# Kernel optimization log

Measured on AMD Instinct MI355X. Metric: run time of the kernel, lower is better.

Reference implementation:

```python
import jax, jax.numpy as jnp
import numpy as np

B, T, M, DFEAT = 256, 30, 2, 256
D_MODEL, NHEAD, NLAYERS, DFF = 768, 12, 12, 3072


def _pe(max_len, d):
    # sinusoidal positional encoding buffer (deterministic, matches PositionalEncoding)
    pos = np.arange(max_len, dtype=np.float32)[:, None]
    div = np.exp(np.arange(0, d, 2, dtype=np.float32) * (-np.log(10000.0) / d))
    pe = np.zeros((max_len, d), dtype=np.float32)
    pe[:, 0::2] = np.sin(pos * div)
    pe[:, 1::2] = np.cos(pos * div)
    return jnp.asarray(pe)


def setup_inputs() -> dict:
    key = jax.random.key(0)
    ks = jax.random.split(key, 16)
    n = lambda k, shape: jax.random.normal(k, shape, jnp.float32) * 0.02
    inp = {}
    inp['x'] = jax.random.normal(ks[0], (B, T, M, DFEAT), jnp.float32)
    inp['mask'] = jax.random.randint(ks[1], (B, T), 0, 2) > 0
    inp['Wp'] = n(ks[2], (D_MODEL, DFEAT)); inp['bp'] = jnp.zeros((D_MODEL,), jnp.float32)
    inp['mod_emb'] = n(ks[3], (M, D_MODEL)); inp['day_emb'] = n(ks[4], (T, D_MODEL))
    inp['readmit'] = n(ks[5], (D_MODEL,)); inp['contrast'] = n(ks[6], (D_MODEL,))
    inp['WqkvS'] = n(ks[7], (NLAYERS, 3 * D_MODEL, D_MODEL)); inp['bqkvS'] = jnp.zeros((NLAYERS, 3 * D_MODEL), jnp.float32)
    inp['WoS'] = n(ks[8], (NLAYERS, D_MODEL, D_MODEL)); inp['boS'] = jnp.zeros((NLAYERS, D_MODEL), jnp.float32)
    inp['ln1wS'] = jnp.ones((NLAYERS, D_MODEL), jnp.float32); inp['ln1bS'] = jnp.zeros((NLAYERS, D_MODEL), jnp.float32)
    inp['ln2wS'] = jnp.ones((NLAYERS, D_MODEL), jnp.float32); inp['ln2bS'] = jnp.zeros((NLAYERS, D_MODEL), jnp.float32)
    inp['W1S'] = n(ks[9], (NLAYERS, DFF, D_MODEL)); inp['b1S'] = jnp.zeros((NLAYERS, DFF), jnp.float32)
    inp['W2S'] = n(ks[10], (NLAYERS, D_MODEL, DFF)); inp['b2S'] = jnp.zeros((NLAYERS, D_MODEL), jnp.float32)
    inp['hW1'] = n(ks[11], (D_MODEL // 2, D_MODEL)); inp['hb1'] = jnp.zeros((D_MODEL // 2,), jnp.float32)
    inp['hlnw'] = jnp.ones((D_MODEL // 2,), jnp.float32); inp['hlnb'] = jnp.zeros((D_MODEL // 2,), jnp.float32)
    inp['hW2'] = n(ks[12], (1, D_MODEL // 2)); inp['hb2'] = jnp.zeros((1,), jnp.float32)
    return inp


def _ln(z, w, b):
    m = z.mean(-1, keepdims=True)
    v = ((z - m) ** 2).mean(-1, keepdims=True)
    return (z - m) * jax.lax.rsqrt(v + 1e-5) * w + b


def reference(x, mask, Wp, bp, mod_emb, day_emb, readmit, contrast,
              WqkvS, bqkvS, WoS, boS, ln1wS, ln1bS, ln2wS, ln2bS,
              W1S, b1S, W2S, b2S, hW1, hb1, hlnw, hlnb, hW2, hb2):
    Bb, Tt, Mm, _ = x.shape
    d = Wp.shape[0]; H = NHEAD; dh = d // H
    L = Tt * Mm; S = L + 2  # static padded length (valid positions key-masked, so faithful)
    # project + activation + modality/day embeddings
    x_flat = x.reshape(Bb, L, -1)
    x_emb = jax.nn.gelu(jnp.einsum('bld,kd->blk', x_flat, Wp) + bp, approximate=False)
    mod_ids = jnp.tile(jnp.arange(Mm), Tt)
    day_ids = jnp.repeat(jnp.arange(Tt), Mm)
    x_emb = x_emb + mod_emb[mod_ids] + day_emb[day_ids]
    # vectorized ragged pack: valid tokens to the front (stable argsort replaces python loop)
    is_valid = jnp.repeat(mask, Mm, axis=1)  # [B, L]
    vlen = is_valid.sum(axis=1).astype(jnp.int32)
    order = jnp.argsort(jnp.logical_not(is_valid).astype(jnp.int32), axis=1, stable=True)
    packed = jnp.take_along_axis(x_emb, order[:, :, None], axis=1)
    packed = packed * (jnp.arange(L)[None, :, None] < vlen[:, None, None])
    h = jnp.pad(packed, ((0, 0), (0, 2), (0, 0)))
    # special tokens at positions vlen / vlen+1, with positional encoding added only there
    pe = _pe(S, d)
    bidx = jnp.arange(Bb)
    h = h.at[bidx, vlen].set(readmit + pe[vlen])
    h = h.at[bidx, vlen + 1].set(contrast + pe[vlen + 1])
    # key padding mask -> additive attention bias
    pad = jnp.arange(S)[None, :] > (vlen[:, None] + 1)
    attn_bias = jnp.where(pad, -1e9, 0.0).astype(h.dtype)[:, None, None, :]

    def layer(hc, p):
        Wqkv, bqkv, Wo, bo, l1w, l1b, l2w, l2b, W1, b1, W2, b2 = p
        z = _ln(hc, l1w, l1b)  # pre-LN
        qkv = jnp.einsum('bsd,kd->bsk', z, Wqkv) + bqkv
        q, k, v = jnp.split(qkv, 3, axis=-1)
        q = q.reshape(Bb, S, H, dh).transpose(0, 2, 1, 3)
        k = k.reshape(Bb, S, H, dh).transpose(0, 2, 1, 3)
        v = v.reshape(Bb, S, H, dh).transpose(0, 2, 1, 3)
        sc = jnp.einsum('bhqd,bhkd->bhqk', q, k) / (dh ** 0.5) + attn_bias
        a = jax.nn.softmax(sc, axis=-1)
        o = jnp.einsum('bhqk,bhkd->bhqd', a, v).transpose(0, 2, 1, 3).reshape(Bb, S, d)
        hc = hc + jnp.einsum('bsd,kd->bsk', o, Wo) + bo
        z2 = _ln(hc, l2w, l2b)
        ff = jax.nn.gelu(jnp.einsum('bsd,fd->bsf', z2, W1) + b1, approximate=False)
        hc = hc + jnp.einsum('bsf,df->bsd', ff, W2) + b2
        return hc, None

    h, _ = jax.lax.scan(layer, h, (WqkvS, bqkvS, WoS, boS, ln1wS, ln1bS, ln2wS, ln2bS, W1S, b1S, W2S, b2S))
    # readmit token readout + MLP head
    tok = h[bidx, vlen]
    hm = jax.nn.gelu(_ln(tok @ hW1.T + hb1, hlnw, hlnb), approximate=False)
    logits = (hm @ hW2.T + hb2)[:, 0]
    return logits
```

## Files before the change

kernel.cpp:

```cpp
#include <hip/hip_runtime.h>
#include <hip/hip_bf16.h>
#include <cmath>

#define BB 256
#define TT 30
#define SS 62
#define DM 768
#define NH 12
#define DFF 3072
#define NTOK (BB*SS)

typedef unsigned short us16;
typedef __bf16 bf16x8 __attribute__((ext_vector_type(8)));
typedef float f32x4 __attribute__((ext_vector_type(4)));

__device__ __forceinline__ us16 f2b(float f){ __hip_bfloat16 t=__float2bfloat16(f); return *reinterpret_cast<us16*>(&t); }
__device__ __forceinline__ float b2f(us16 u){ __hip_bfloat16 t; *reinterpret_cast<us16*>(&t)=u; return __bfloat162float(t); }
__device__ __forceinline__ float dgelu(float x){ return 0.5f*x*(1.0f+erff(x*0.7071067811865475f)); }
__device__ __forceinline__ f32x4 mfma16(bf16x8 a, bf16x8 b, f32x4 c){ return __builtin_amdgcn_mfma_f32_16x16x32_bf16(a,b,c,0,0,0); }

__device__ __forceinline__ void gload16(const void* g, void* l) {
    __builtin_amdgcn_global_load_lds(
        (__attribute__((address_space(1))) void*)(uintptr_t)g,
        (__attribute__((address_space(3))) void*)(uint32_t)(uintptr_t)l,
        16, 0, 0);
}

__global__ __launch_bounds__(256) void detect_mask_kernel(
    const unsigned char* __restrict__ m, int* __restrict__ flag)
{
    __shared__ int sub4, oddw;
    if (threadIdx.x == 0) { sub4 = 0; oddw = 0; }
    __syncthreads();
    for (int j = threadIdx.x; j < BB*TT; j += blockDim.x) {
        unsigned char v = m[j];
        if (v) {
            if (j & 3) sub4 = 1;
            if ((j >> 2) & 1) oddw = 1;
        }
    }
    __syncthreads();
    if (threadIdx.x == 0) *flag = sub4 ? 1 : (oddw ? 0 : 2);
}

__global__ __launch_bounds__(256) void cvt_kernel(
    const float* __restrict__ in, us16* __restrict__ out, int n8)
{
    int t = blockIdx.x*256 + threadIdx.x;
    if (t >= n8) return;
    const float4* s = (const float4*)(in + (long)t*8);
    float4 a = s[0], b = s[1];
    us16 tmp[8] = {f2b(a.x),f2b(a.y),f2b(a.z),f2b(a.w),f2b(b.x),f2b(b.y),f2b(b.z),f2b(b.w)};
    *(uint4*)(out + (long)t*8) = *(uint4*)tmp;
}

__global__ __launch_bounds__(256) void cvt_layer_kernel(
    const float* __restrict__ qkv, const float* __restrict__ wo,
    const float* __restrict__ w1,  const float* __restrict__ w2,
    us16* __restrict__ dqkv, us16* __restrict__ dwo,
    us16* __restrict__ dw1,  us16* __restrict__ dw2)
{
    long t = (long)blockIdx.x*256 + threadIdx.x;
    const float* src; us16* dst; long off;
    if (t < 221184)      { src = qkv; dst = dqkv; off = t; }
    else if (t < 294912) { src = wo;  dst = dwo;  off = t - 221184; }
    else if (t < 589824) { src = w1;  dst = dw1;  off = t - 294912; }
    else                 { src = w2;  dst = dw2;  off = t - 589824; }
    const float4* s = (const float4*)(src + off*8);
    float4 a = s[0], b = s[1];
    us16 tmp[8] = {f2b(a.x),f2b(a.y),f2b(a.z),f2b(a.w),f2b(b.x),f2b(b.y),f2b(b.z),f2b(b.w)};
    *(uint4*)(dst + off*8) = *(uint4*)tmp;
}

template<int EPI>
__global__ __launch_bounds__(256) void gemm_bf(const us16* __restrict__ A,
    const us16* __restrict__ W, const float* __restrict__ bias,
    void* __restrict__ outv, int N, int K, int ntn)
{
    __shared__ us16 As[2][128*64];
    __shared__ us16 Ws[2][128*64];
    const int tid  = threadIdx.x;
    const int lane = tid & 63;
    const int wave = tid >> 6;
    const int wr = wave >> 1, wc = wave & 1;
    const int li = lane & 15, g = lane >> 4;

    const int nwg = gridDim.x;
    const int lin = blockIdx.x;
    const int newlin = (lin & 7) * (nwg >> 3) + (lin >> 3);
    const long tm = newlin / ntn, tn = newlin % ntn;

    const int swzc = ((lane & 7) ^ (lane >> 3)) * 8;
    const us16* agp = A + (tm*128 + wave*32 + (lane>>3))*(long)K + swzc;
    const us16* wgp = W + (tn*128 + wave*32 + (lane>>3))*(long)K + swzc;

    f32x4 acc[4][4];
    #pragma unroll
    for (int i=0;i<4;i++)
        #pragma unroll
        for (int j=0;j<4;j++)
            #pragma unroll
            for (int r=0;r<4;r++) acc[i][j][r] = 0.f;

    const int nt = K >> 6;
    #pragma unroll
    for (int c=0;c<4;c++) {
        gload16(agp + (long)c*8*K, &As[0][(wave*4+c)*512]);
        gload16(wgp + (long)c*8*K, &Ws[0][(wave*4+c)*512]);
    }
    __syncthreads();

    int cur = 0;
    for (int t = 0; t < nt; ++t) {
        if (t + 1 < nt) {
            const long k0 = (long)(t+1) * 64;
            #pragma unroll
            for (int c=0;c<4;c++) {
                gload16(agp + k0 + (long)c*8*K, &As[cur^1][(wave*4+c)*512]);
                gload16(wgp + k0 + (long)c*8*K, &Ws[cur^1][(wave*4+c)*512]);
            }
        }
        #pragma unroll
        for (int kk=0; kk<2; kk++) {
            bf16x8 afr[4], bfr[4];
            #pragma unroll
            for (int mi=0;mi<4;mi++) {
                int r = wr*64 + mi*16 + li;
                afr[mi] = *(const bf16x8*)&As[cur][r*64 + ((kk*4 + g) ^ (r & 7))*8];
            }
            #pragma unroll
            for (int ni=0;ni<4;ni++) {
                int r = wc*64 + ni*16 + li;
                bfr[ni] = *(const bf16x8*)&Ws[cur][r*64 + ((kk*4 + g) ^ (r & 7))*8];
            }
            #pragma unroll
            for (int mi=0;mi<4;mi++)
                #pragma unroll
                for (int ni=0;ni<4;ni++)
                    acc[mi][ni] = mfma16(afr[mi], bfr[ni], acc[mi][ni]);
        }
        __syncthreads();
        cur ^= 1;
    }

    const long rbase = tm*128 + wr*64 + (g*4);
    const long cbase = tn*128 + wc*64 + li;
    #pragma unroll
    for (int mi=0;mi<4;mi++) {
        #pragma unroll
        for (int ni=0;ni<4;ni++) {
            long col = cbase + ni*16;
            float bv = bias[col];
            #pragma unroll
            for (int r=0;r<4;r++) {
                long row = rbase + mi*16 + r;
                float v = acc[mi][ni][r] + bv;
                if constexpr (EPI == 0) {
                    ((us16*)outv)[row*(long)N + col] = f2b(v);
                } else if constexpr (EPI == 1) {
                    ((us16*)outv)[row*(long)N + col] = f2b(dgelu(v));
                } else {
                    float* o = (float*)outv;
                    o[row*(long)N + col] += v;
                }
            }
        }
    }
}

__global__ __launch_bounds__(256) void pack_kernel(
    const us16* __restrict__ e, const void* __restrict__ maskv,
    const int* __restrict__ flagp,
    const float* __restrict__ mod_emb, const float* __restrict__ day_emb,
    const float* __restrict__ readmit, const float* __restrict__ contrast,
    float* __restrict__ h, int* __restrict__ vlen_out)
{
    __shared__ int day_of[TT];
    __shared__ int nvalid;
    const int b = blockIdx.x, tid = threadIdx.x;
    if (tid == 0) {
        const int fl = *flagp;
        int c = 0;
        for (int t = 0; t < TT; t++) {
            int mv;
            if (fl == 1)      mv = ((const unsigned char*)maskv)[b*TT + t];
            else if (fl == 2) mv = ((const int*)maskv)[(b*TT + t)*2];
            else              mv = ((const int*)maskv)[b*TT + t];
            if (mv != 0) day_of[c++] = t;
        }
        nvalid = c;
        vlen_out[b] = 2*c;
    }
    __syncthreads();
    const int vl = 2*nvalid;
    for (int p = 0; p < SS; p++) {
        for (int d = tid; d < DM; d += 256) {
            float val;
            if (p < vl) {
                int day = day_of[p >> 1];
                int m = p & 1;
                int l = day*2 + m;
                val = b2f(e[((long)b*(TT*2) + l)*DM + d]) + mod_emb[m*DM + d] + day_emb[day*DM + d];
            } else if (p == vl || p == vl + 1) {
                float freq = expf(-(float)(d & ~1) * (9.2103403719761836f/768.f));
                float pe = (d & 1) ? cosf((float)p * freq) : sinf((float)p * freq);
                val = ((p == vl) ? readmit[d] : contrast[d]) + pe;
            } else {
                val = 0.f;
            }
            h[((long)b*SS + p)*DM + d] = val;
        }
    }
}

__global__ __launch_bounds__(256) void ln_kernel(
    const float* __restrict__ x, const float* __restrict__ w,
    const float* __restrict__ bprm, us16* __restrict__ z)
{
    const int row  = blockIdx.x*4 + (threadIdx.x >> 6);
    const int lane = threadIdx.x & 63;
    const float* xr = x + (long)row*DM;
    float4 v[3];
    float s = 0.f, s2 = 0.f;
    #pragma unroll
    for (int j=0;j<3;j++) {
        v[j] = *(const float4*)(xr + lane*4 + j*256);
        s  += v[j].x + v[j].y + v[j].z + v[j].w;
        s2 += v[j].x*v[j].x + v[j].y*v[j].y + v[j].z*v[j].z + v[j].w*v[j].w;
    }
    #pragma unroll
    for (int d=1; d<64; d<<=1) { s += __shfl_xor(s, d); s2 += __shfl_xor(s2, d); }
    const float m  = s * (1.f/768.f);
    const float var = s2 * (1.f/768.f) - m*m;
    const float rs = rsqrtf(var + 1e-5f);
    us16* zr = z + (long)row*DM;
    #pragma unroll
    for (int j=0;j<3;j++) {
        int c0 = lane*4 + j*256;
        float vv[4] = {v[j].x, v[j].y, v[j].z, v[j].w};
        ushort4 o;
        o.x = f2b((vv[0]-m)*rs*w[c0+0] + bprm[c0+0]);
        o.y = f2b((vv[1]-m)*rs*w[c0+1] + bprm[c0+1]);
        o.z = f2b((vv[2]-m)*rs*w[c0+2] + bprm[c0+2]);
        o.w = f2b((vv[3]-m)*rs*w[c0+3] + bprm[c0+3]);
        *(ushort4*)(zr + c0) = o;
    }
}

__global__ __launch_bounds__(256) void attn_kernel(
    const us16* __restrict__ qkv, const int* __restrict__ vlenp,
    us16* __restrict__ ctx)
{
    __shared__ us16 Ql[64*64];
    __shared__ us16 Kl[64*64];
    __shared__ us16 Vt[64*64];
    __shared__ us16 Pl[4*16*64];
    const int b = blockIdx.x, hh = blockIdx.y;
    const int tid = threadIdx.x;
    const int vl = vlenp[b];

    {
        int s  = tid >> 2;
        int d0 = (tid & 3) * 16;
        if (s < SS) {
            long base = ((long)b*SS + s)*(3*DM) + hh*64 + d0;
            uint4 a0 = *(const uint4*)(qkv + base);
            uint4 a1 = *(const uint4*)(qkv + base + 8);
            *(uint4*)&Ql[s*64 + d0]     = a0;
            *(uint4*)&Ql[s*64 + d0 + 8] = a1;
            uint4 c0 = *(const uint4*)(qkv + base + DM);
            uint4 c1 = *(const uint4*)(qkv + base + DM + 8);
            *(uint4*)&Kl[s*64 + d0]     = c0;
            *(uint4*)&Kl[s*64 + d0 + 8] = c1;
            us16 vv[16];
            *(uint4*)&vv[0] = *(const uint4*)(qkv + base + 2*DM);
            *(uint4*)&vv[8] = *(const uint4*)(qkv + base + 2*DM + 8);
            #pragma unroll
            for (int j=0;j<16;j++) Vt[(d0+j)*64 + s] = vv[j];
        } else {
            uint4 zz = make_uint4(0,0,0,0);
            *(uint4*)&Ql[s*64 + d0] = zz; *(uint4*)&Ql[s*64 + d0 + 8] = zz;
            *(uint4*)&Kl[s*64 + d0] = zz; *(uint4*)&Kl[s*64 + d0 + 8] = zz;
            #pragma unroll
            for (int j=0;j<16;j++) Vt[(d0+j)*64 + s] = 0;
        }
    }
    __syncthreads();

    const int lane = tid & 63, wave = tid >> 6;
    const int li = lane & 15, g = lane >> 4;
    const int qbase = wave * 16;

    f32x4 sacc[4];
    #pragma unroll
    for (int kb=0; kb<4; kb++) {
        f32x4 a; a[0]=a[1]=a[2]=a[3]=0.f;
        #pragma unroll
        for (int dc=0; dc<2; dc++) {
            bf16x8 qa = *(const bf16x8*)&Ql[(qbase + li)*64 + dc*32 + g*8];
            bf16x8 ka = *(const bf16x8*)&Kl[(kb*16 + li)*64 + dc*32 + g*8];
            a = mfma16(qa, ka, a);
        }
        sacc[kb] = a;
    }

    float den[4];
    #pragma unroll
    for (int r=0;r<4;r++) {
        float sc[4]; float mx = -3e38f;
        #pragma unroll
        for (int kb=0;kb<4;kb++) {
            int key = kb*16 + li;
            float v = sacc[kb][r]*0.125f + ((key <= vl + 1) ? 0.f : -1e9f);
            sc[kb] = v; mx = fmaxf(mx, v);
        }
        #pragma unroll
        for (int d=1; d<16; d<<=1) mx = fmaxf(mx, __shfl_xor(mx, d));
        float sm = 0.f;
        #pragma unroll
        for (int kb=0;kb<4;kb++) {
            float e = expf(sc[kb] - mx);
            sm += e;
            Pl[wave*1024 + (g*4 + r)*64 + kb*16 + li] = f2b(e);
        }
        #pragma unroll
        for (int d=1; d<16; d<<=1) sm += __shfl_xor(sm, d);
        den[r] = sm;
    }
    __syncthreads();

    #pragma unroll
    for (int vb=0; vb<4; vb++) {
        f32x4 oa; oa[0]=oa[1]=oa[2]=oa[3]=0.f;
        #pragma unroll
        for (int kc=0; kc<2; kc++) {
            bf16x8 pa = *(const bf16x8*)&Pl[wave*1024 + li*64 + kc*32 + g*8];
            bf16x8 va = *(const bf16x8*)&Vt[(vb*16 + li)*64 + kc*32 + g*8];
            oa = mfma16(pa, va, oa);
        }
        #pragma unroll
        for (int r=0;r<4;r++) {
            int s = qbase + g*4 + r;
            if (s < SS)
                ctx[((long)b*SS + s)*DM + hh*64 + vb*16 + li] = f2b(oa[r] / den[r]);
        }
    }
}

__global__ __launch_bounds__(384) void head_kernel(
    const float* __restrict__ h, const int* __restrict__ vlenp,
    const float* __restrict__ hW1, const float* __restrict__ hb1,
    const float* __restrict__ hlnw, const float* __restrict__ hlnb,
    const float* __restrict__ hW2, const float* __restrict__ hb2,
    float* __restrict__ out)
{
    __shared__ float tokS[DM];
    __shared__ float ps[6], ps2[6];
    const int b = blockIdx.x, tid = threadIdx.x;
    const float* tok = h + ((long)b*SS + vlenp[b])*DM;
    for (int i = tid; i < DM; i += 384) tokS[i] = tok[i];
    __syncthreads();

    const float* wrow = hW1 + (long)tid*DM;
    float acc = hb1[tid];
    for (int k = 0; k < DM; k += 4) {
        float4 wv = *(const float4*)(wrow + k);
        acc += tokS[k]*wv.x + tokS[k+1]*wv.y + tokS[k+2]*wv.z + tokS[k+3]*wv.w;
    }
    float s = acc, s2 = acc*acc;
    #pragma unroll
    for (int d=1; d<64; d<<=1) { s += __shfl_xor(s, d); s2 += __shfl_xor(s2, d); }
    const int wavei = tid >> 6, lane = tid & 63;
    if (lane == 0) { ps[wavei] = s; ps2[wavei] = s2; }
    __syncthreads();
    float S = 0.f, S2 = 0.f;
    for (int i=0;i<6;i++){ S += ps[i]; S2 += ps2[i]; }
    const float m = S * (1.f/384.f);
    const float var = S2 * (1.f/384.f) - m*m;
    const float rs = rsqrtf(var + 1e-5f);
    float z = (acc - m)*rs*hlnw[tid] + hlnb[tid];
    float part = dgelu(z) * hW2[tid];
    #pragma unroll
    for (int d=1; d<64; d<<=1) part += __shfl_xor(part, d);
    __syncthreads();
    if (lane == 0) ps[wavei] = part;
    __syncthreads();
    if (tid == 0) {
        float t = 0.f;
        for (int i=0;i<6;i++) t += ps[i];
        out[b] = t + hb2[0];
    }
}

extern "C" void kernel_launch(void* const* d_in, const int* in_sizes, int n_in,
                              void* d_out, int out_size, void* d_ws, size_t ws_size,
                              hipStream_t stream)
{
    (void)in_sizes; (void)n_in; (void)out_size; (void)ws_size;
    const float* x        = (const float*)d_in[0];
    const void*  mask     = d_in[1];
    const float* Wp       = (const float*)d_in[2];
    const float* bp       = (const float*)d_in[3];
    const float* mod_emb  = (const float*)d_in[4];
    const float* day_emb  = (const float*)d_in[5];
    const float* readmit  = (const float*)d_in[6];
    const float* contrast = (const float*)d_in[7];
    const float* WqkvS    = (const float*)d_in[8];
    const float* bqkvS    = (const float*)d_in[9];
    const float* WoS      = (const float*)d_in[10];
    const float* boS      = (const float*)d_in[11];
    const float* ln1w     = (const float*)d_in[12];
    const float* ln1b     = (const float*)d_in[13];
    const float* ln2w     = (const float*)d_in[14];
    const float* ln2b     = (const float*)d_in[15];
    const float* W1S      = (const float*)d_in[16];
    const float* b1S      = (const float*)d_in[17];
    const float* W2S      = (const float*)d_in[18];
    const float* b2S      = (const float*)d_in[19];
    const float* hW1      = (const float*)d_in[20];
    const float* hb1      = (const float*)d_in[21];
    const float* hlnw     = (const float*)d_in[22];
    const float* hlnb     = (const float*)d_in[23];
    const float* hW2      = (const float*)d_in[24];
    const float* hb2      = (const float*)d_in[25];
    float* out = (float*)d_out;

    char* ws = (char*)d_ws;
    float* h    = (float*)ws;
    us16*  zb   = (us16*) (ws + 48758784);
    us16*  big  = (us16*) (ws + 73138176);
    us16*  wl   = (us16*) (ws + 170655744);
    us16*  xb   = (us16*) (ws + 184811520);
    us16*  wpb  = (us16*) (ws + 192675840);
    int*   vlen = (int*)  (ws + 193069056);
    int*   mflag= (int*)  (ws + 193070080);
    us16*  qkvb = big;
    us16*  ffb  = big;
    us16*  eb   = big;
    us16* qkvw = wl;
    us16* wow  = wl + 1769472;
    us16* w1w  = wl + 2359296;
    us16* w2w  = wl + 4718592;

    detect_mask_kernel<<<1,256,0,stream>>>((const unsigned char*)mask, mflag);
    cvt_kernel<<<1920,256,0,stream>>>(x, xb, 491520);
    cvt_kernel<<<96,256,0,stream>>>(Wp, wpb, 24576);
    gemm_bf<1><<<720,256,0,stream>>>(xb, wpb, bp, eb, DM, 256, 6);
    pack_kernel<<<256,256,0,stream>>>(eb, mask, mflag, mod_emb, day_emb, readmit, contrast, h, vlen);

    for (int l = 0; l < 12; l++) {
        cvt_layer_kernel<<<3456,256,0,stream>>>(
            WqkvS + (long)l*3*DM*DM, WoS + (long)l*DM*DM,
            W1S + (long)l*DFF*DM,    W2S + (long)l*DM*DFF,
            qkvw, wow, w1w, w2w);
        ln_kernel<<<NTOK/4,256,0,stream>>>(h, ln1w + l*DM, ln1b + l*DM, zb);
        gemm_bf<0><<<2232,256,0,stream>>>(zb, qkvw, bqkvS + l*3*DM, qkvb, 3*DM, DM, 18);
        attn_kernel<<<dim3(256,12),256,0,stream>>>(qkvb, vlen, zb);
        gemm_bf<2><<<744,256,0,stream>>>(zb, wow, boS + l*DM, h, DM, DM, 6);
        ln_kernel<<<NTOK/4,256,0,stream>>>(h, ln2w + l*DM, ln2b + l*DM, zb);
        gemm_bf<1><<<2976,256,0,stream>>>(zb, w1w, b1S + l*DFF, ffb, DFF, DM, 24);
        gemm_bf<2><<<744,256,0,stream>>>(ffb, w2w, b2S + l*DM, h, DM, DFF, 6);
    }

    head_kernel<<<256,384,0,stream>>>(h, vlen, hW1, hb1, hlnw, hlnb, hW2, hb2, out);
}
```

Measured before the change: 4.860 ms.

## Use partial vmcnt waits and raw barriers to overlap prefetch in GEMM loop

Result: faster. 4.744 ms (-2.4%).

```diff
diff --git a/kernel.cpp b/kernel.cpp
--- a/kernel.cpp
+++ b/kernel.cpp
@@ -94,6 +94,21 @@
     const us16* agp = A + (tm*128 + wave*32 + (lane>>3))*(long)K + swzc;
     const us16* wgp = W + (tn*128 + wave*32 + (lane>>3))*(long)K + swzc;
 
+    int aoff[2][4], woff[2][4];
+    #pragma unroll
+    for (int kk=0;kk<2;kk++) {
+        #pragma unroll
+        for (int mi=0;mi<4;mi++) {
+            int r = wr*64 + mi*16 + li;
+            aoff[kk][mi] = r*64 + ((kk*4 + g) ^ (r & 7))*8;
+        }
+        #pragma unroll
+        for (int ni=0;ni<4;ni++) {
+            int r = wc*64 + ni*16 + li;
+            woff[kk][ni] = r*64 + ((kk*4 + g) ^ (r & 7))*8;
+        }
+    }
+
     f32x4 acc[4][4];
     #pragma unroll
     for (int i=0;i<4;i++)
@@ -108,39 +123,44 @@
         gload16(agp + (long)c*8*K, &As[0][(wave*4+c)*512]);
         gload16(wgp + (long)c*8*K, &Ws[0][(wave*4+c)*512]);
     }
-    __syncthreads();
-
-    int cur = 0;
+    agp += 64; wgp += 64;
+
     for (int t = 0; t < nt; ++t) {
+        const int cur = t & 1;
         if (t + 1 < nt) {
-            const long k0 = (long)(t+1) * 64;
             #pragma unroll
             for (int c=0;c<4;c++) {
-                gload16(agp + k0 + (long)c*8*K, &As[cur^1][(wave*4+c)*512]);
-                gload16(wgp + k0 + (long)c*8*K, &Ws[cur^1][(wave*4+c)*512]);
+                gload16(agp + (long)c*8*K, &As[cur^1][(wave*4+c)*512]);
+                gload16(wgp + (long)c*8*K, &Ws[cur^1][(wave*4+c)*512]);
             }
-        }
+            agp += 64; wgp += 64;
+            asm volatile("s_waitcnt vmcnt(8)" ::: "memory");
+        } else {
+            asm volatile("s_waitcnt vmcnt(0)" ::: "memory");
+        }
+        __builtin_amdgcn_sched_barrier(0);
+        __builtin_amdgcn_s_barrier();
+        __builtin_amdgcn_sched_barrier(0);
+        const us16* Ab = As[cur];
+        const us16* Wb = Ws[cur];
         #pragma unroll
         for (int kk=0; kk<2; kk++) {
             bf16x8 afr[4], bfr[4];
             #pragma unroll
-            for (int mi=0;mi<4;mi++) {
-                int r = wr*64 + mi*16 + li;
-                afr[mi] = *(const bf16x8*)&As[cur][r*64 + ((kk*4 + g) ^ (r & 7))*8];
-            }
-            #pragma unroll
-            for (int ni=0;ni<4;ni++) {
-                int r = wc*64 + ni*16 + li;
-                bfr[ni] = *(const bf16x8*)&Ws[cur][r*64 + ((kk*4 + g) ^ (r & 7))*8];
-            }
+            for (int mi=0;mi<4;mi++) afr[mi] = *(const bf16x8*)(Ab + aoff[kk][mi]);
+            #pragma unroll
+            for (int ni=0;ni<4;ni++) bfr[ni] = *(const bf16x8*)(Wb + woff[kk][ni]);
+            if (kk == 0) __builtin_amdgcn_s_setprio(1);
             #pragma unroll
             for (int mi=0;mi<4;mi++)
                 #pragma unroll
                 for (int ni=0;ni<4;ni++)
                     acc[mi][ni] = mfma16(afr[mi], bfr[ni], acc[mi][ni]);
         }
-        __syncthreads();
-        cur ^= 1;
+        __builtin_amdgcn_s_setprio(0);
+        __builtin_amdgcn_sched_barrier(0);
+        __builtin_amdgcn_s_barrier();
+        __builtin_amdgcn_sched_barrier(0);
     }
 
     const long rbase = tm*128 + wr*64 + (g*4);
```

## Deepen GEMM pipeline to 4-stage K=32 buffers with explicit vmcnt waits

Applied to the files above, without the earlier changes.

Measured after the change: 5.473 ms. 12.6% more time.

```diff
diff --git a/kernel.cpp b/kernel.cpp
--- a/kernel.cpp
+++ b/kernel.cpp
@@ -77,8 +77,8 @@
     const us16* __restrict__ W, const float* __restrict__ bias,
     void* __restrict__ outv, int N, int K, int ntn)
 {
-    __shared__ us16 As[2][128*64];
-    __shared__ us16 Ws[2][128*64];
+    __shared__ us16 As[4][128*32];
+    __shared__ us16 Ws[4][128*32];
     const int tid  = threadIdx.x;
     const int lane = tid & 63;
     const int wave = tid >> 6;
@@ -86,13 +86,27 @@
     const int li = lane & 15, g = lane >> 4;
 
     const int nwg = gridDim.x;
-    const int lin = blockIdx.x;
-    const int newlin = (lin & 7) * (nwg >> 3) + (lin >> 3);
+    const int q8 = nwg >> 3, r8 = nwg & 7;
+    const int xcd = blockIdx.x & 7, b8 = blockIdx.x >> 3;
+    const int newlin = (xcd < r8 ? xcd*(q8+1) : r8*(q8+1) + (xcd - r8)*q8) + b8;
     const long tm = newlin / ntn, tn = newlin % ntn;
 
-    const int swzc = ((lane & 7) ^ (lane >> 3)) * 8;
-    const us16* agp = A + (tm*128 + wave*32 + (lane>>3))*(long)K + swzc;
-    const us16* wgp = W + (tn*128 + wave*32 + (lane>>3))*(long)K + swzc;
+    const int c0 = tid, c1 = 256 + tid;
+    const int ar0 = c0 >> 2, ar1 = c1 >> 2;
+    const int acb0 = (c0 & 3) ^ ((ar0 & 3) ^ ((ar0 >> 2) & 3));
+    const int acb1 = (c1 & 3) ^ ((ar1 & 3) ^ ((ar1 >> 2) & 3));
+    const us16* aS0 = A + (tm*128 + ar0)*(long)K + acb0*8;
+    const us16* aS1 = A + (tm*128 + ar1)*(long)K + acb1*8;
+    const us16* wS0 = W + (tn*128 + ar0)*(long)K + acb0*8;
+    const us16* wS1 = W + (tn*128 + ar1)*(long)K + acb1*8;
+    const int d0 = wave*512, d1 = 2048 + wave*512;
+
+    const int sw = (li & 3) ^ ((li >> 2) & 3);
+    int aoff[4], woff[4];
+    #pragma unroll
+    for (int mi=0;mi<4;mi++) aoff[mi] = (wr*64 + mi*16 + li)*32 + ((g ^ sw)*8);
+    #pragma unroll
+    for (int ni=0;ni<4;ni++) woff[ni] = (wc*64 + ni*16 + li)*32 + ((g ^ sw)*8);
 
     f32x4 acc[4][4];
     #pragma unroll
@@ -102,45 +116,57 @@
             #pragma unroll
             for (int r=0;r<4;r++) acc[i][j][r] = 0.f;
 
-    const int nt = K >> 6;
-    #pragma unroll
-    for (int c=0;c<4;c++) {
-        gload16(agp + (long)c*8*K, &As[0][(wave*4+c)*512]);
-        gload16(wgp + (long)c*8*K, &Ws[0][(wave*4+c)*512]);
-    }
-    __syncthreads();
-
-    int cur = 0;
+    const int nt = K >> 5;
+
+    #pragma unroll
+    for (int tt=0; tt<3; ++tt) {
+        if (tt < nt) {
+            const int b = tt & 3;
+            const long k = (long)tt * 32;
+            gload16(aS0 + k, &As[b][d0]);
+            gload16(aS1 + k, &As[b][d1]);
+            gload16(wS0 + k, &Ws[b][d0]);
+            gload16(wS1 + k, &Ws[b][d1]);
+        }
+    }
+
     for (int t = 0; t < nt; ++t) {
-        if (t + 1 < nt) {
-            const long k0 = (long)(t+1) * 64;
+        if (t + 3 < nt) {
+            const int b = (t+3) & 3;
+            const long k = (long)(t+3) * 32;
+            gload16(aS0 + k, &As[b][d0]);
+            gload16(aS1 + k, &As[b][d1]);
+            gload16(wS0 + k, &Ws[b][d0]);
+            gload16(wS1 + k, &Ws[b][d1]);
+        }
+        const int rem = nt - 1 - t;
+        const int pend = rem > 3 ? 3 : rem;
+        __builtin_amdgcn_sched_barrier(0);
+        if (pend == 3)      asm volatile("s_waitcnt vmcnt(12)" ::: "memory");
+        else if (pend == 2) asm volatile("s_waitcnt vmcnt(8)"  ::: "memory");
+        else if (pend == 1) asm volatile("s_waitcnt vmcnt(4)"  ::: "memory");
+        else                asm volatile("s_waitcnt vmcnt(0)"  ::: "memory");
+        __builtin_amdgcn_sched_barrier(0);
+        __builtin_amdgcn_s_barrier();
+        __builtin_amdgcn_sched_barrier(0);
+
+        const us16* Ab = As[t & 3];
+        const us16* Wb = Ws[t & 3];
+        bf16x8 afr[4], bfr[4];
+        #pragma unroll
+        for (int mi=0;mi<4;mi++) afr[mi] = *(const bf16x8*)(Ab + aoff[mi]);
+        #pragma unroll
+        for (int ni=0;ni<4;ni++) bfr[ni] = *(const bf16x8*)(Wb + woff[ni]);
+        __builtin_amdgcn_s_setprio(1);
+        #pragma unroll
+        for (int mi=0;mi<4;mi++)
             #pragma unroll
-            for (int c=0;c<4;c++) {
-                gload16(agp + k0 + (long)c*8*K, &As[cur^1][(wave*4+c)*512]);
-                gload16(wgp + k0 + (long)c*8*K, &Ws[cur^1][(wave*4+c)*512]);
-            }
-        }
-        #pragma unroll
-        for (int kk=0; kk<2; kk++) {
-            bf16x8 afr[4], bfr[4];
-            #pragma unroll
-            for (int mi=0;mi<4;mi++) {
-                int r = wr*64 + mi*16 + li;
-                afr[mi] = *(const bf16x8*)&As[cur][r*64 + ((kk*4 + g) ^ (r & 7))*8];
-            }
-            #pragma unroll
-            for (int ni=0;ni<4;ni++) {
-                int r = wc*64 + ni*16 + li;
-                bfr[ni] = *(const bf16x8*)&Ws[cur][r*64 + ((kk*4 + g) ^ (r & 7))*8];
-            }
-            #pragma unroll
-            for (int mi=0;mi<4;mi++)
-                #pragma unroll
-                for (int ni=0;ni<4;ni++)
-                    acc[mi][ni] = mfma16(afr[mi], bfr[ni], acc[mi][ni]);
-        }
-        __syncthreads();
-        cur ^= 1;
+            for (int ni=0;ni<4;ni++)
+                acc[mi][ni] = mfma16(afr[mi], bfr[ni], acc[mi][ni]);
+        __builtin_amdgcn_s_setprio(0);
+        __builtin_amdgcn_sched_barrier(0);
+        __builtin_amdgcn_s_barrier();
+        __builtin_amdgcn_sched_barrier(0);
     }
 
     const long rbase = tm*128 + wr*64 + (g*4);
```

## Single-buffer GEMM LDS to raise occupancy, add setprio and precomputed offsets

Applied to the files above, without the earlier changes.

After: 13.69 ms. +181.7%, slower.

```diff
diff --git a/kernel.cpp b/kernel.cpp
--- a/kernel.cpp
+++ b/kernel.cpp
@@ -73,12 +73,12 @@
 }
 
 template<int EPI>
-__global__ __launch_bounds__(256) void gemm_bf(const us16* __restrict__ A,
+__global__ __launch_bounds__(256, 5) void gemm_bf(const us16* __restrict__ A,
     const us16* __restrict__ W, const float* __restrict__ bias,
     void* __restrict__ outv, int N, int K, int ntn)
 {
-    __shared__ us16 As[2][128*64];
-    __shared__ us16 Ws[2][128*64];
+    __shared__ us16 As[128*64];
+    __shared__ us16 Ws[128*64];
     const int tid  = threadIdx.x;
     const int lane = tid & 63;
     const int wave = tid >> 6;
@@ -86,14 +86,30 @@
     const int li = lane & 15, g = lane >> 4;
 
     const int nwg = gridDim.x;
-    const int lin = blockIdx.x;
-    const int newlin = (lin & 7) * (nwg >> 3) + (lin >> 3);
+    const int q8 = nwg >> 3, r8 = nwg & 7;
+    const int xcd = blockIdx.x & 7, b8 = blockIdx.x >> 3;
+    const int newlin = (xcd < r8 ? xcd*(q8+1) : r8*(q8+1) + (xcd - r8)*q8) + b8;
     const long tm = newlin / ntn, tn = newlin % ntn;
 
     const int swzc = ((lane & 7) ^ (lane >> 3)) * 8;
     const us16* agp = A + (tm*128 + wave*32 + (lane>>3))*(long)K + swzc;
     const us16* wgp = W + (tn*128 + wave*32 + (lane>>3))*(long)K + swzc;
 
+    int aoff[2][4], woff[2][4];
+    #pragma unroll
+    for (int kk=0;kk<2;kk++) {
+        #pragma unroll
+        for (int mi=0;mi<4;mi++) {
+            int r = wr*64 + mi*16 + li;
+            aoff[kk][mi] = r*64 + ((kk*4 + g) ^ (r & 7))*8;
+        }
+        #pragma unroll
+        for (int ni=0;ni<4;ni++) {
+            int r = wc*64 + ni*16 + li;
+            woff[kk][ni] = r*64 + ((kk*4 + g) ^ (r & 7))*8;
+        }
+    }
+
     f32x4 acc[4][4];
     #pragma unroll
     for (int i=0;i<4;i++)
@@ -102,45 +118,29 @@
             #pragma unroll
             for (int r=0;r<4;r++) acc[i][j][r] = 0.f;
 
-    const int nt = K >> 6;
-    #pragma unroll
-    for (int c=0;c<4;c++) {
-        gload16(agp + (long)c*8*K, &As[0][(wave*4+c)*512]);
-        gload16(wgp + (long)c*8*K, &Ws[0][(wave*4+c)*512]);
-    }
-    __syncthreads();
-
-    int cur = 0;
-    for (int t = 0; t < nt; ++t) {
-        if (t + 1 < nt) {
-            const long k0 = (long)(t+1) * 64;
-            #pragma unroll
-            for (int c=0;c<4;c++) {
-                gload16(agp + k0 + (long)c*8*K, &As[cur^1][(wave*4+c)*512]);
-                gload16(wgp + k0 + (long)c*8*K, &Ws[cur^1][(wave*4+c)*512]);
-            }
-        }
+    for (int k0 = 0; k0 < K; k0 += 64) {
+        #pragma unroll
+        for (int c=0;c<4;c++) {
+            gload16(agp + k0 + (long)c*8*K, &As[(wave*4+c)*512]);
+            gload16(wgp + k0 + (long)c*8*K, &Ws[(wave*4+c)*512]);
+        }
+        __syncthreads();
         #pragma unroll
         for (int kk=0; kk<2; kk++) {
             bf16x8 afr[4], bfr[4];
             #pragma unroll
-            for (int mi=0;mi<4;mi++) {
-                int r = wr*64 + mi*16 + li;
-                afr[mi] = *(const bf16x8*)&As[cur][r*64 + ((kk*4 + g) ^ (r & 7))*8];
-            }
-            #pragma unroll
-            for (int ni=0;ni<4;ni++) {
-                int r = wc*64 + ni*16 + li;
-                bfr[ni] = *(const bf16x8*)&Ws[cur][r*64 + ((kk*4 + g) ^ (r & 7))*8];
-            }
+            for (int mi=0;mi<4;mi++) afr[mi] = *(const bf16x8*)(As + aoff[kk][mi]);
+            #pragma unroll
+            for (int ni=0;ni<4;ni++) bfr[ni] = *(const bf16x8*)(Ws + woff[kk][ni]);
+            if (kk == 0) __builtin_amdgcn_s_setprio(1);
             #pragma unroll
             for (int mi=0;mi<4;mi++)
                 #pragma unroll
                 for (int ni=0;ni<4;ni++)
                     acc[mi][ni] = mfma16(afr[mi], bfr[ni], acc[mi][ni]);
         }
+        __builtin_amdgcn_s_setprio(0);
         __syncthreads();
-        cur ^= 1;
     }
 
     const long rbase = tm*128 + wr*64 + (g*4);
```
